# Performance work log

Hardware: AMD Instinct MI355X
Metric: run time of the kernel (lower is better)

Reference implementation:

```python
import jax, jax.numpy as jnp
import numpy as np

B, T, D, H = 4, 4096, 2048, 128

def setup_inputs() -> dict:
    key = jax.random.key(0)
    k1, k2, k3, k4 = jax.random.split(key, 4)
    scale = 0.02
    return {
        "x": jax.random.normal(k1, (B, T, D), dtype=jnp.float32),
        "Wq": jax.random.normal(k2, (D, H), dtype=jnp.float32) * scale,
        "Wk": jax.random.normal(k3, (D, H), dtype=jnp.float32) * scale,
        "Wv": jax.random.normal(k4, (D, H), dtype=jnp.float32) * scale,
    }

def reference(x, Wq, Wk, Wv):
    # x: [B,T,D]; projections to [B,T,H]
    q = jnp.einsum('btd,dh->bth', x, Wq)
    k = jnp.einsum('btd,dh->bth', x, Wk)
    v = jnp.einsum('btd,dh->bth', x, Wv)
    scale = 1.0 / jnp.sqrt(jnp.asarray(q.shape[-1], q.dtype))
    scores = jnp.einsum('bth,bsh->bts', q, k) * scale  # [B,T,T]
    t = x.shape[1]
    causal = jnp.tril(jnp.ones((t, t), dtype=bool))
    scores = jnp.where(causal, scores, -jnp.inf)
    weights = jax.nn.softmax(scores, axis=-1)
    # dropout p=0.0 (eval) -> identity
    out = jnp.einsum('bts,bsh->bth', weights, v)
    return out
```

## Files before the change

kernel.cpp:

```cpp
#include <hip/hip_runtime.h>
#include <hip/hip_bf16.h>

#define Bq 4
#define Tq 4096
#define Dq 2048
#define Hq 128
#define Mq (Bq*Tq)
#define CHUNK 16

typedef __attribute__((ext_vector_type(8))) short bf16x8;
typedef __attribute__((ext_vector_type(4))) float f32x4;

static __device__ __forceinline__ short bfbits(float f) {
    union { __hip_bfloat16 h; short s; } u;
    u.h = __float2bfloat16(f);
    return u.s;
}
static __device__ __forceinline__ float bf2f(short s) {
    union { unsigned u; float f; } v;
    v.u = ((unsigned)(unsigned short)s) << 16;
    return v.f;
}
#define WAIT_LDS() __builtin_amdgcn_s_waitcnt(0xC07F)

static __device__ __forceinline__ void gload16(const void* g, void* l) {
    __builtin_amdgcn_global_load_lds(
        (const __attribute__((address_space(1))) unsigned int*)g,
        (__attribute__((address_space(3))) unsigned int*)l, 16, 0, 0);
}

__global__ __launch_bounds__(256, 1) void wt_kernel(
    const float* __restrict__ Wqp,
    const float* __restrict__ Wkp,
    const float* __restrict__ Wvp,
    short* __restrict__ wTg)
{
    __shared__ short trsp[128][136];
    const int kc = blockIdx.x;
    const int w  = blockIdx.y;
    const float* __restrict__ W = (w == 0) ? Wqp : (w == 1) ? Wkp : Wvp;
    const float scale = (w == 0) ? 0.08838834764831843f : 1.0f;
    const int t = threadIdx.x;

    #pragma unroll
    for (int i = 0; i < 16; i++) {
        int idx = t + i * 256;
        int r = idx >> 5, c4 = idx & 31;
        float4 f = *(const float4*)&W[(size_t)(kc * 128 + r) * Hq + c4 * 4];
        trsp[c4 * 4 + 0][r] = bfbits(f.x * scale);
        trsp[c4 * 4 + 1][r] = bfbits(f.y * scale);
        trsp[c4 * 4 + 2][r] = bfbits(f.z * scale);
        trsp[c4 * 4 + 3][r] = bfbits(f.w * scale);
    }
    __syncthreads();
    #pragma unroll
    for (int i = 0; i < 8; i++) {
        int idx = t + i * 256;
        int h = idx >> 4, c8 = idx & 15;
        *(bf16x8*)&wTg[((size_t)w * 128 + h) * Dq + kc * 128 + c8 * 8] =
            *(bf16x8*)&trsp[h][c8 * 8];
    }
}

__global__ __launch_bounds__(512, 2) void qkv_fused_kernel(
    const float* __restrict__ x,
    const short* __restrict__ wTg,
    short* __restrict__ qg,
    short* __restrict__ kg,
    short* __restrict__ vTt)
{
    __shared__ __attribute__((aligned(128))) char smem[114688];

    const int bid  = blockIdx.x;
    const int mi   = bid & 127;
    const int ni   = bid >> 7;
    const int m0   = mi * 128;
    const int n0   = ni * 192;

    const int t    = threadIdx.x;
    const int l    = t & 63;
    const int w    = t >> 6;
    const int l15  = l & 15;
    const int quad = l >> 4;
    const int wmi  = w & 3;
    const int wni  = w >> 2;
    const int swzA = l15 << 4;
    const int swzB = (l15 & 7) << 4;

    f32x4 o[2][6];
    #pragma unroll
    for (int mf = 0; mf < 2; mf++)
        #pragma unroll
        for (int j = 0; j < 6; j++) o[mf][j] = (f32x4){0.f, 0.f, 0.f, 0.f};

    const short* wsrc0 = wTg + (size_t)(n0 + 24 * w + (l >> 3)) * Dq
                             + (((l & 7) ^ (l >> 3)) << 3);

    #define ISSUE(it2, par)                                                      \
        do {                                                                     \
            char* wb_ = smem + (par) * 24576;                                    \
            _Pragma("unroll")                                                    \
            for (int j = 0; j < 3; j++)                                          \
                gload16(wsrc0 + (size_t)j * 8 * Dq + (it2) * 64,                 \
                        wb_ + (w * 3 + j) * 1024);                               \
            char* xb_ = smem + 49152 + (par) * 32768;                            \
            _Pragma("unroll")                                                    \
            for (int j = 0; j < 4; j++) {                                        \
                int row_ = 16 * w + 4 * j + (l >> 4);                            \
                int col_ = ((l & 15) ^ (4 * j + (l >> 4))) << 2;                 \
                gload16(x + (size_t)(m0 + row_) * Dq + (it2) * 64 + col_,        \
                        xb_ + (w * 4 + j) * 1024);                               \
            }                                                                    \
        } while (0)

    #define COMPUTE(par)                                                         \
        do {                                                                     \
            const char* wb_ = smem + (par) * 24576;                              \
            const char* xb_ = smem + 49152 + (par) * 32768;                      \
            _Pragma("unroll")                                                    \
            for (int kk = 0; kk < 2; kk++) {                                     \
                bf16x8 a[2], b[6];                                               \
                _Pragma("unroll")                                                \
                for (int mf = 0; mf < 2; mf++) {                                 \
                    const char* rp = xb_ + (wmi * 32 + mf * 16 + l15) * 256;     \
                    const int kb = kk * 128 + quad * 32;                         \
                    f32x4 f0 = *(const f32x4*)(rp + ((kb     ) ^ swzA));         \
                    f32x4 f1 = *(const f32x4*)(rp + ((kb + 16) ^ swzA));         \
                    bf16x8 af;                                                   \
                    af[0] = bfbits(f0[0]); af[1] = bfbits(f0[1]);                \
                    af[2] = bfbits(f0[2]); af[3] = bfbits(f0[3]);                \
                    af[4] = bfbits(f1[0]); af[5] = bfbits(f1[1]);                \
                    af[6] = bfbits(f1[2]); af[7] = bfbits(f1[3]);                \
                    a[mf] = af;                                                  \
                }                                                                \
                _Pragma("unroll")                                                \
                for (int j = 0; j < 6; j++)                                      \
                    b[j] = *(const bf16x8*)(wb_ + (wni * 96 + j * 16 + l15) * 128\
                                                + ((kk * 64 + quad * 16) ^ swzB));\
                _Pragma("unroll")                                                \
                for (int mf = 0; mf < 2; mf++)                                   \
                    _Pragma("unroll")                                            \
                    for (int j = 0; j < 6; j++)                                  \
                        o[mf][j] = __builtin_amdgcn_mfma_f32_16x16x32_bf16(      \
                            a[mf], b[j], o[mf][j], 0, 0, 0);                     \
            }                                                                    \
        } while (0)

    ISSUE(0, 0);
    ISSUE(1, 1);

    #pragma unroll 1
    for (int it = 0; it < 32; ++it) {
        if (it < 31) asm volatile("s_waitcnt vmcnt(7)" ::: "memory");
        else         asm volatile("s_waitcnt vmcnt(0)" ::: "memory");
        __builtin_amdgcn_s_barrier();
        __builtin_amdgcn_sched_barrier(0);
        COMPUTE(it & 1);
        __builtin_amdgcn_s_barrier();
        __builtin_amdgcn_sched_barrier(0);
        if (it < 30) ISSUE(it + 2, it & 1);
    }

    #undef COMPUTE
    #undef ISSUE

    {
        short (*e)[200] = (short(*)[200])smem;
        #pragma unroll
        for (int mf = 0; mf < 2; mf++)
            #pragma unroll
            for (int j = 0; j < 6; j++) {
                int nloc = wni * 96 + j * 16;
                if (n0 + nloc < 256) {
                    #pragma unroll
                    for (int reg = 0; reg < 4; reg++)
                        e[wmi * 32 + mf * 16 + quad * 4 + reg][nloc + l15] =
                            bfbits(o[mf][j][reg]);
                }
            }
        __syncthreads();
        const int r  = t >> 2;
        const int u0 = (t & 3) * 6;
        #pragma unroll
        for (int i = 0; i < 6; i++) {
            int u  = u0 + i;
            int ng = n0 + u * 8;
            if (ng < 256) {
                bf16x8 val = *(bf16x8*)&e[r][u * 8];
                short* dst = (ng < 128) ? &qg[(size_t)(m0 + r) * Hq + ng]
                                        : &kg[(size_t)(m0 + r) * Hq + (ng - 128)];
                *(bf16x8*)dst = val;
            }
        }
    }
    if (ni == 1) {
        __syncthreads();
        short (*ev)[136] = (short(*)[136])(smem + 53248);
        #pragma unroll
        for (int mf = 0; mf < 2; mf++)
            #pragma unroll
            for (int j = 0; j < 6; j++) {
                int nloc = wni * 96 + j * 16;
                if (nloc >= 64) {
                    short4 pk;
                    pk.x = bfbits(o[mf][j][0]); pk.y = bfbits(o[mf][j][1]);
                    pk.z = bfbits(o[mf][j][2]); pk.w = bfbits(o[mf][j][3]);
                    *(short4*)&ev[(nloc - 64) + l15][wmi * 32 + mf * 16 + quad * 4] = pk;
                }
            }
        __syncthreads();
        const int bb  = m0 / Tq;
        const int jt0 = (m0 % Tq) >> 6;
        #pragma unroll
        for (int i = 0; i < 4; i++) {
            int idx = t + i * 512;
            int h = idx >> 4, u = idx & 15;
            int m = u * 8;
            int jt = jt0 + (m >> 6);
            *(bf16x8*)&vTt[(((size_t)bb * (Tq / 64) + jt) * 128 + h) * 64 + (m & 63)] =
                *(bf16x8*)&ev[h][m];
        }
    }
}

__global__ __launch_bounds__(256, 3) void attn_part_kernel(
    const short* __restrict__ qg, const short* __restrict__ kg,
    const short* __restrict__ vTt,
    short* __restrict__ Opart,
    float* __restrict__ lv)
{
    __shared__ short ks_s[64][136];
    __shared__ short vt_s[128][72];
    __shared__ short ps_s[64][72];

    const int qt = blockIdx.x;
    const int b  = blockIdx.y;
    const int c  = blockIdx.z;
    const int q0 = qt * 64;

    const int lo = c * CHUNK;
    const int hi = min(qt + 1, lo + CHUNK);
    if (lo >= hi) return;

    const int t    = threadIdx.x;
    const int lane = t & 63;
    const int qw   = t >> 6;
    const int l15  = lane & 15;
    const int quad = lane >> 4;

    bf16x8 qf[4];
    {
        const short* qsrc = qg + (size_t)(b * Tq + q0 + qw * 16 + l15) * Hq + quad * 8;
        #pragma unroll
        for (int kk = 0; kk < 4; kk++)
            qf[kk] = *(const bf16x8*)(qsrc + kk * 32);
    }

    float lsum[4] = {0.f, 0.f, 0.f, 0.f};
    f32x4 o[8];
    #pragma unroll
    for (int nf = 0; nf < 8; nf++) o[nf] = (f32x4){0.f, 0.f, 0.f, 0.f};

    bf16x8 kreg[4], vreg[4];
    {
        const size_t kbase = (size_t)(b * Tq + lo * 64) * Hq;
        const short* vsrc = vTt + (((size_t)b * (Tq / 64) + lo) * 128) * 64;
        #pragma unroll
        for (int i = 0; i < 4; i++) {
            int idx = t + i * 256;
            kreg[i] = *(const bf16x8*)&kg[kbase + (size_t)(idx >> 4) * Hq + (idx & 15) * 8];
            vreg[i] = *(const bf16x8*)&vsrc[idx * 8];
        }
        #pragma unroll
        for (int i = 0; i < 4; i++) {
            int idx = t + i * 256;
            *(bf16x8*)&ks_s[idx >> 4][(idx & 15) * 8] = kreg[i];
            *(bf16x8*)&vt_s[idx >> 3][(idx & 7) * 8]  = vreg[i];
        }
    }
    __syncthreads();

    for (int jt = lo; jt < hi; jt++) {
        if (jt + 1 < hi) {
            const size_t kbase = (size_t)(b * Tq + (jt + 1) * 64) * Hq;
            const short* vsrc = vTt + (((size_t)b * (Tq / 64) + jt + 1) * 128) * 64;
            #pragma unroll
            for (int i = 0; i < 4; i++) {
                int idx = t + i * 256;
                kreg[i] = *(const bf16x8*)&kg[kbase + (size_t)(idx >> 4) * Hq + (idx & 15) * 8];
                vreg[i] = *(const bf16x8*)&vsrc[idx * 8];
            }
        }

        f32x4 sacc[4];
        #pragma unroll
        for (int nf = 0; nf < 4; nf++) sacc[nf] = (f32x4){0.f, 0.f, 0.f, 0.f};
        #pragma unroll
        for (int kk = 0; kk < 4; kk++) {
            bf16x8 bk[4];
            #pragma unroll
            for (int nf = 0; nf < 4; nf++)
                bk[nf] = *(bf16x8*)&ks_s[nf * 16 + l15][kk * 32 + quad * 8];
            #pragma unroll
            for (int nf = 0; nf < 4; nf++)
                sacc[nf] = __builtin_amdgcn_mfma_f32_16x16x32_bf16(qf[kk], bk[nf], sacc[nf], 0, 0, 0);
        }

        const bool diag = (jt == qt);
        #pragma unroll
        for (int reg = 0; reg < 4; reg++) {
            const int rloc = qw * 16 + quad * 4 + reg;
            #pragma unroll
            for (int nf = 0; nf < 4; nf++) {
                float s = sacc[nf][reg];
                if (diag && (nf * 16 + l15 > rloc)) s = -1e30f;
                float p = __expf(s);
                lsum[reg] += p;
                ps_s[rloc][nf * 16 + l15] = bfbits(p);
            }
        }
        WAIT_LDS();

        #pragma unroll
        for (int ks2 = 0; ks2 < 2; ks2++) {
            bf16x8 ap = *(bf16x8*)&ps_s[qw * 16 + l15][ks2 * 32 + quad * 8];
            bf16x8 bv[8];
            #pragma unroll
            for (int nf = 0; nf < 8; nf++)
                bv[nf] = *(bf16x8*)&vt_s[nf * 16 + l15][ks2 * 32 + quad * 8];
            #pragma unroll
            for (int nf = 0; nf < 8; nf++)
                o[nf] = __builtin_amdgcn_mfma_f32_16x16x32_bf16(ap, bv[nf], o[nf], 0, 0, 0);
        }

        __syncthreads();
        if (jt + 1 < hi) {
            #pragma unroll
            for (int i = 0; i < 4; i++) {
                int idx = t + i * 256;
                *(bf16x8*)&ks_s[idx >> 4][(idx & 15) * 8] = kreg[i];
                *(bf16x8*)&vt_s[idx >> 3][(idx & 7) * 8]  = vreg[i];
            }
            __syncthreads();
        }
    }

    #pragma unroll
    for (int reg = 0; reg < 4; reg++) {
        #pragma unroll
        for (int mm = 8; mm >= 1; mm >>= 1)
            lsum[reg] += __shfl_xor(lsum[reg], mm, 16);
    }
    const size_t zoff = (size_t)c * Mq;
    if (l15 == 0) {
        #pragma unroll
        for (int reg = 0; reg < 4; reg++)
            lv[zoff + (size_t)b * Tq + q0 + qw * 16 + quad * 4 + reg] = lsum[reg];
    }

    __syncthreads();
    short (*epi)[136] = (short(*)[136])&ks_s[0][0];
    #pragma unroll
    for (int nf = 0; nf < 8; nf++)
        #pragma unroll
        for (int reg = 0; reg < 4; reg++)
            epi[qw * 16 + quad * 4 + reg][nf * 16 + l15] = bfbits(o[nf][reg]);
    __syncthreads();
    #pragma unroll
    for (int i = 0; i < 4; i++) {
        int idx = t + i * 256;
        int r = idx >> 4, cc = idx & 15;
        *(bf16x8*)&Opart[(zoff + (size_t)b * Tq + q0 + r) * Hq + cc * 8] =
            *(bf16x8*)&epi[r][cc * 8];
    }
}

__global__ __launch_bounds__(256, 4) void merge_kernel(
    const short* __restrict__ Opart, const float* __restrict__ lv,
    float* __restrict__ outg)
{
    const int t   = threadIdx.x;
    const int row = blockIdx.x * 16 + (t >> 4);
    const int cu  = t & 15;

    const int rl  = row & (Tq - 1);
    const int nch = (rl >> 10) + 1;

    float lsum = 0.f;
    float acc[8] = {};
    for (int cc = 0; cc < nch; cc++) {
        lsum += lv[(size_t)cc * Mq + row];
        bf16x8 oc = *(const bf16x8*)&Opart[((size_t)cc * Mq + row) * Hq + cu * 8];
        #pragma unroll
        for (int j = 0; j < 8; j++) acc[j] += bf2f(oc[j]);
    }
    float inv = 1.0f / lsum;

    float4 r0, r1;
    r0.x = acc[0] * inv; r0.y = acc[1] * inv; r0.z = acc[2] * inv; r0.w = acc[3] * inv;
    r1.x = acc[4] * inv; r1.y = acc[5] * inv; r1.z = acc[6] * inv; r1.w = acc[7] * inv;
    float* dst = &outg[(size_t)row * Hq + cu * 8];
    *(float4*)dst       = r0;
    *(float4*)(dst + 4) = r1;
}

extern "C" void kernel_launch(void* const* d_in, const int* in_sizes, int n_in,
                              void* d_out, int out_size, void* d_ws, size_t ws_size,
                              hipStream_t stream) {
    const float* x   = (const float*)d_in[0];
    const float* Wqp = (const float*)d_in[1];
    const float* Wkp = (const float*)d_in[2];
    const float* Wvp = (const float*)d_in[3];
    float* out = (float*)d_out;

    short* qg    = (short*)d_ws;
    short* kg    = qg  + (size_t)Mq * Hq;
    short* vTt   = kg  + (size_t)Mq * Hq;
    short* Opart = vTt + (size_t)Mq * Hq;
    short* wTg   = Opart;
    float* lv    = (float*)(Opart + (size_t)4 * Mq * Hq);

    wt_kernel<<<dim3(16, 3), dim3(256), 0, stream>>>(Wqp, Wkp, Wvp, wTg);
    qkv_fused_kernel<<<dim3(256), dim3(512), 0, stream>>>(x, wTg, qg, kg, vTt);
    attn_part_kernel<<<dim3(Tq / 64, Bq, 4), dim3(256), 0, stream>>>(qg, kg, vTt, Opart, lv);
    merge_kernel<<<dim3(Mq / 16), dim3(256), 0, stream>>>(Opart, lv, out);
}
```

Measured before the change: 265.2 us.

## Stage QKV projection loads through registers and convert x to bf16 before LDS

The QKV projection GEMM no longer uses direct global-to-LDS loads. x and W tiles are now loaded into registers two iterations ahead, x is converted to bf16 once per element, and the packed bf16 data is written to swizzled LDS. This halves the LDS footprint for x (114688 to 81920 bytes) and removes the repeated fp32-to-bf16 conversion the consumer waves did in the MFMA loop. In exchange it adds register pressure, costs VGPR-to-LDS write instructions, and changes the barrier and waitcnt schedule, with an unrolled two-stage loop and epilogue.

```diff
diff --git a/kernel.cpp b/kernel.cpp
--- a/kernel.cpp
+++ b/kernel.cpp
@@ -21,13 +21,11 @@
     v.u = ((unsigned)(unsigned short)s) << 16;
     return v.f;
 }
+static __device__ __forceinline__ unsigned pk2(float a, float b) {
+    return ((unsigned)(unsigned short)bfbits(a)) |
+           (((unsigned)(unsigned short)bfbits(b)) << 16);
+}
 #define WAIT_LDS() __builtin_amdgcn_s_waitcnt(0xC07F)
-
-static __device__ __forceinline__ void gload16(const void* g, void* l) {
-    __builtin_amdgcn_global_load_lds(
-        (const __attribute__((address_space(1))) unsigned int*)g,
-        (__attribute__((address_space(3))) unsigned int*)l, 16, 0, 0);
-}
 
 __global__ __launch_bounds__(256, 1) void wt_kernel(
     const float* __restrict__ Wqp,
@@ -69,7 +67,7 @@
     short* __restrict__ kg,
     short* __restrict__ vTt)
 {
-    __shared__ __attribute__((aligned(128))) char smem[114688];
+    __shared__ __attribute__((aligned(128))) char smem[81920];
 
     const int bid  = blockIdx.x;
     const int mi   = bid & 127;
@@ -84,8 +82,7 @@
     const int quad = l >> 4;
     const int wmi  = w & 3;
     const int wni  = w >> 2;
-    const int swzA = l15 << 4;
-    const int swzB = (l15 & 7) << 4;
+    const int swz  = (l15 & 7) << 4;
 
     f32x4 o[2][6];
     #pragma unroll
@@ -93,50 +90,56 @@
         #pragma unroll
         for (int j = 0; j < 6; j++) o[mf][j] = (f32x4){0.f, 0.f, 0.f, 0.f};
 
-    const short* wsrc0 = wTg + (size_t)(n0 + 24 * w + (l >> 3)) * Dq
-                             + (((l & 7) ^ (l >> 3)) << 3);
-
-    #define ISSUE(it2, par)                                                      \
+    const float* xsrc = x + (size_t)(m0 + (t >> 4)) * Dq + (t & 15) * 4;
+    const short* wsrc = wTg + (size_t)(n0 + (t >> 3)) * Dq + (t & 7) * 8;
+    const int xwb0 = (t >> 4) * 128 + (((t & 15) << 3) ^ (((t >> 4) & 7) << 4));
+    const int wwb0 = (t >> 3) * 128 + (((t & 7) << 4) ^ (((t >> 3) & 7) << 4));
+
+    float4  xg[2][4];
+    bf16x8  wg[2][3];
+
+    #define LOAD(it2, s)                                                         \
+        do {                                                                     \
+            _Pragma("unroll")                                                    \
+            for (int j = 0; j < 4; j++)                                          \
+                xg[s][j] = *(const float4*)(xsrc + (size_t)j * 32 * Dq + (it2) * 64); \
+            _Pragma("unroll")                                                    \
+            for (int j = 0; j < 3; j++)                                          \
+                wg[s][j] = *(const bf16x8*)(wsrc + (size_t)j * 64 * Dq + (it2) * 64); \
+        } while (0)
+
+    #define WRITE(par, s)                                                        \
         do {                                                                     \
             char* wb_ = smem + (par) * 24576;                                    \
+            char* xb_ = smem + 49152 + (par) * 16384;                            \
+            _Pragma("unroll")                                                    \
+            for (int j = 0; j < 4; j++) {                                        \
+                uint2 u;                                                         \
+                u.x = pk2(xg[s][j].x, xg[s][j].y);                               \
+                u.y = pk2(xg[s][j].z, xg[s][j].w);                               \
+                *(uint2*)(xb_ + xwb0 + j * 4096) = u;                            \
+            }                                                                    \
             _Pragma("unroll")                                                    \
             for (int j = 0; j < 3; j++)                                          \
-                gload16(wsrc0 + (size_t)j * 8 * Dq + (it2) * 64,                 \
-                        wb_ + (w * 3 + j) * 1024);                               \
-            char* xb_ = smem + 49152 + (par) * 32768;                            \
-            _Pragma("unroll")                                                    \
-            for (int j = 0; j < 4; j++) {                                        \
-                int row_ = 16 * w + 4 * j + (l >> 4);                            \
-                int col_ = ((l & 15) ^ (4 * j + (l >> 4))) << 2;                 \
-                gload16(x + (size_t)(m0 + row_) * Dq + (it2) * 64 + col_,        \
-                        xb_ + (w * 4 + j) * 1024);                               \
-            }                                                                    \
+                *(bf16x8*)(wb_ + wwb0 + j * 8192) = wg[s][j];                    \
         } while (0)
 
     #define COMPUTE(par)                                                         \
         do {                                                                     \
             const char* wb_ = smem + (par) * 24576;                              \
-            const char* xb_ = smem + 49152 + (par) * 32768;                      \
+            const char* xb_ = smem + 49152 + (par) * 16384;                      \
             _Pragma("unroll")                                                    \
             for (int kk = 0; kk < 2; kk++) {                                     \
+                const int kb = kk * 64 + quad * 16;                              \
                 bf16x8 a[2], b[6];                                               \
                 _Pragma("unroll")                                                \
-                for (int mf = 0; mf < 2; mf++) {                                 \
-                    const char* rp = xb_ + (wmi * 32 + mf * 16 + l15) * 256;     \
-                    const int kb = kk * 128 + quad * 32;                         \
-                    f32x4 f0 = *(const f32x4*)(rp + ((kb     ) ^ swzA));         \
-                    f32x4 f1 = *(const f32x4*)(rp + ((kb + 16) ^ swzA));         \
-                    bf16x8 af;                                                   \
-                    af[0] = bfbits(f0[0]); af[1] = bfbits(f0[1]);                \
-                    af[2] = bfbits(f0[2]); af[3] = bfbits(f0[3]);                \
-                    af[4] = bfbits(f1[0]); af[5] = bfbits(f1[1]);                \
-                    af[6] = bfbits(f1[2]); af[7] = bfbits(f1[3]);                \
-                    a[mf] = af;                                                  \
-                }                                                                \
+                for (int mf = 0; mf < 2; mf++)                                   \
+                    a[mf] = *(const bf16x8*)(xb_ + (wmi * 32 + mf * 16 + l15) * 128 \
+                                                 + (kb ^ swz));                  \
                 _Pragma("unroll")                                                \
                 for (int j = 0; j < 6; j++)                                      \
                     b[j] = *(const bf16x8*)(wb_ + (wni * 96 + j * 16 + l15) * 128\
-                                                + ((kk * 64 + quad * 16) ^ swzB));\
+                                                + (kb ^ swz));                   \
                 _Pragma("unroll")                                                \
                 for (int mf = 0; mf < 2; mf++)                                   \
                     _Pragma("unroll")                                            \
@@ -146,23 +149,46 @@
             }                                                                    \
         } while (0)
 
-    ISSUE(0, 0);
-    ISSUE(1, 1);
+    #define BODY(it, p)                                                          \
+        do {                                                                     \
+            asm volatile("s_waitcnt lgkmcnt(0)" ::: "memory");                   \
+            __builtin_amdgcn_s_barrier();                                        \
+            __builtin_amdgcn_sched_barrier(0);                                   \
+            LOAD((it) + 2, p);                                                   \
+            COMPUTE(p);                                                          \
+            asm volatile("s_waitcnt vmcnt(7)" ::: "memory");                     \
+            __builtin_amdgcn_sched_barrier(0);                                   \
+            WRITE(1 - (p), 1 - (p));                                             \
+        } while (0)
+
+    LOAD(0, 0);
+    LOAD(1, 1);
+    asm volatile("s_waitcnt vmcnt(7)" ::: "memory");
+    __builtin_amdgcn_sched_barrier(0);
+    WRITE(0, 0);
 
     #pragma unroll 1
-    for (int it = 0; it < 32; ++it) {
-        if (it < 31) asm volatile("s_waitcnt vmcnt(7)" ::: "memory");
-        else         asm volatile("s_waitcnt vmcnt(0)" ::: "memory");
-        __builtin_amdgcn_s_barrier();
-        __builtin_amdgcn_sched_barrier(0);
-        COMPUTE(it & 1);
-        __builtin_amdgcn_s_barrier();
-        __builtin_amdgcn_sched_barrier(0);
-        if (it < 30) ISSUE(it + 2, it & 1);
-    }
-
+    for (int itp = 0; itp < 15; itp++) {
+        BODY(itp * 2,     0);
+        BODY(itp * 2 + 1, 1);
+    }
+    asm volatile("s_waitcnt lgkmcnt(0)" ::: "memory");
+    __builtin_amdgcn_s_barrier();
+    __builtin_amdgcn_sched_barrier(0);
+    COMPUTE(0);
+    asm volatile("s_waitcnt vmcnt(0)" ::: "memory");
+    __builtin_amdgcn_sched_barrier(0);
+    WRITE(1, 1);
+    asm volatile("s_waitcnt lgkmcnt(0)" ::: "memory");
+    __builtin_amdgcn_s_barrier();
+    __builtin_amdgcn_sched_barrier(0);
+    COMPUTE(1);
+    __builtin_amdgcn_s_barrier();
+
+    #undef BODY
     #undef COMPUTE
-    #undef ISSUE
+    #undef WRITE
+    #undef LOAD
 
     {
         short (*e)[200] = (short(*)[200])smem;
@@ -195,7 +221,7 @@
     }
     if (ni == 1) {
         __syncthreads();
-        short (*ev)[136] = (short(*)[136])(smem + 53248);
+        short (*ev)[136] = (short(*)[136])smem;
         #pragma unroll
         for (int mf = 0; mf < 2; mf++)
             #pragma unroll
```

Result: slower. 285.9 us (+7.8%).

## Replace LDS-staged QKV GEMM with direct global loads and split-K across waves

Applied to the files above, without the earlier changes.

The QKV projection kernel no longer stages x and W tiles through LDS with async global_load_lds and double buffering. Each wave now loads its MFMA operands straight from global memory into registers. The K dimension is split across wave pairs, and the two partial results are combined through a small LDS reduction before the epilogue. This removes LDS traffic, the per-iteration barriers and a large LDS footprint, at the cost of uncoalesced, latency-exposed global loads, no explicit prefetch, and a doubled per-wave accumulator register set.

```diff
diff --git a/kernel.cpp b/kernel.cpp
--- a/kernel.cpp
+++ b/kernel.cpp
@@ -22,12 +22,6 @@
     return v.f;
 }
 #define WAIT_LDS() __builtin_amdgcn_s_waitcnt(0xC07F)
-
-static __device__ __forceinline__ void gload16(const void* g, void* l) {
-    __builtin_amdgcn_global_load_lds(
-        (const __attribute__((address_space(1))) unsigned int*)g,
-        (__attribute__((address_space(3))) unsigned int*)l, 16, 0, 0);
-}
 
 __global__ __launch_bounds__(256, 1) void wt_kernel(
     const float* __restrict__ Wqp,
@@ -69,7 +63,7 @@
     short* __restrict__ kg,
     short* __restrict__ vTt)
 {
-    __shared__ __attribute__((aligned(128))) char smem[114688];
+    __shared__ __attribute__((aligned(128))) char smem[51200];
 
     const int bid  = blockIdx.x;
     const int mi   = bid & 127;
@@ -82,102 +76,88 @@
     const int w    = t >> 6;
     const int l15  = l & 15;
     const int quad = l >> 4;
-    const int wmi  = w & 3;
-    const int wni  = w >> 2;
-    const int swzA = l15 << 4;
-    const int swzB = (l15 & 7) << 4;
-
-    f32x4 o[2][6];
-    #pragma unroll
-    for (int mf = 0; mf < 2; mf++)
+    const int wm   = (w >> 2) & 1;
+    const int wk   = (w >> 1) & 1;
+    const int wn   = w & 1;
+
+    const float* xp = x + (size_t)(m0 + wm * 64 + l15) * Dq + wk * 1024 + quad * 8;
+    const short* wp = wTg + (size_t)(n0 + wn * 96 + l15) * Dq + wk * 1024 + quad * 8;
+
+    f32x4 o[4][6];
+    #pragma unroll
+    for (int mf = 0; mf < 4; mf++)
         #pragma unroll
         for (int j = 0; j < 6; j++) o[mf][j] = (f32x4){0.f, 0.f, 0.f, 0.f};
 
-    const short* wsrc0 = wTg + (size_t)(n0 + 24 * w + (l >> 3)) * Dq
-                             + (((l & 7) ^ (l >> 3)) << 3);
-
-    #define ISSUE(it2, par)                                                      \
-        do {                                                                     \
-            char* wb_ = smem + (par) * 24576;                                    \
-            _Pragma("unroll")                                                    \
-            for (int j = 0; j < 3; j++)                                          \
-                gload16(wsrc0 + (size_t)j * 8 * Dq + (it2) * 64,                 \
-                        wb_ + (w * 3 + j) * 1024);                               \
-            char* xb_ = smem + 49152 + (par) * 32768;                            \
-            _Pragma("unroll")                                                    \
-            for (int j = 0; j < 4; j++) {                                        \
-                int row_ = 16 * w + 4 * j + (l >> 4);                            \
-                int col_ = ((l & 15) ^ (4 * j + (l >> 4))) << 2;                 \
-                gload16(x + (size_t)(m0 + row_) * Dq + (it2) * 64 + col_,        \
-                        xb_ + (w * 4 + j) * 1024);                               \
-            }                                                                    \
-        } while (0)
-
-    #define COMPUTE(par)                                                         \
-        do {                                                                     \
-            const char* wb_ = smem + (par) * 24576;                              \
-            const char* xb_ = smem + 49152 + (par) * 32768;                      \
-            _Pragma("unroll")                                                    \
-            for (int kk = 0; kk < 2; kk++) {                                     \
-                bf16x8 a[2], b[6];                                               \
-                _Pragma("unroll")                                                \
-                for (int mf = 0; mf < 2; mf++) {                                 \
-                    const char* rp = xb_ + (wmi * 32 + mf * 16 + l15) * 256;     \
-                    const int kb = kk * 128 + quad * 32;                         \
-                    f32x4 f0 = *(const f32x4*)(rp + ((kb     ) ^ swzA));         \
-                    f32x4 f1 = *(const f32x4*)(rp + ((kb + 16) ^ swzA));         \
-                    bf16x8 af;                                                   \
-                    af[0] = bfbits(f0[0]); af[1] = bfbits(f0[1]);                \
-                    af[2] = bfbits(f0[2]); af[3] = bfbits(f0[3]);                \
-                    af[4] = bfbits(f1[0]); af[5] = bfbits(f1[1]);                \
-                    af[6] = bfbits(f1[2]); af[7] = bfbits(f1[3]);                \
-                    a[mf] = af;                                                  \
-                }                                                                \
-                _Pragma("unroll")                                                \
-                for (int j = 0; j < 6; j++)                                      \
-                    b[j] = *(const bf16x8*)(wb_ + (wni * 96 + j * 16 + l15) * 128\
-                                                + ((kk * 64 + quad * 16) ^ swzB));\
-                _Pragma("unroll")                                                \
-                for (int mf = 0; mf < 2; mf++)                                   \
-                    _Pragma("unroll")                                            \
-                    for (int j = 0; j < 6; j++)                                  \
-                        o[mf][j] = __builtin_amdgcn_mfma_f32_16x16x32_bf16(      \
-                            a[mf], b[j], o[mf][j], 0, 0, 0);                     \
-            }                                                                    \
-        } while (0)
-
-    ISSUE(0, 0);
-    ISSUE(1, 1);
-
-    #pragma unroll 1
+    #pragma unroll 2
     for (int it = 0; it < 32; ++it) {
-        if (it < 31) asm volatile("s_waitcnt vmcnt(7)" ::: "memory");
-        else         asm volatile("s_waitcnt vmcnt(0)" ::: "memory");
-        __builtin_amdgcn_s_barrier();
-        __builtin_amdgcn_sched_barrier(0);
-        COMPUTE(it & 1);
-        __builtin_amdgcn_s_barrier();
-        __builtin_amdgcn_sched_barrier(0);
-        if (it < 30) ISSUE(it + 2, it & 1);
-    }
-
-    #undef COMPUTE
-    #undef ISSUE
+        const int k0 = it * 32;
+        bf16x8 a[4];
+        #pragma unroll
+        for (int mf = 0; mf < 4; mf++) {
+            float4 f0 = *(const float4*)(xp + (size_t)mf * 16 * Dq + k0);
+            float4 f1 = *(const float4*)(xp + (size_t)mf * 16 * Dq + k0 + 4);
+            bf16x8 af;
+            af[0] = bfbits(f0.x); af[1] = bfbits(f0.y);
+            af[2] = bfbits(f0.z); af[3] = bfbits(f0.w);
+            af[4] = bfbits(f1.x); af[5] = bfbits(f1.y);
+            af[6] = bfbits(f1.z); af[7] = bfbits(f1.w);
+            a[mf] = af;
+        }
+        bf16x8 b[6];
+        #pragma unroll
+        for (int j = 0; j < 6; j++)
+            b[j] = *(const bf16x8*)(wp + (size_t)j * 16 * Dq + k0);
+        #pragma unroll
+        for (int mf = 0; mf < 4; mf++)
+            #pragma unroll
+            for (int j = 0; j < 6; j++)
+                o[mf][j] = __builtin_amdgcn_mfma_f32_16x16x32_bf16(
+                    a[mf], b[j], o[mf][j], 0, 0, 0);
+    }
+
+    {
+        float* cmb = (float*)smem;
+        const int widx = wm * 2 + wn;
+        #pragma unroll
+        for (int p = 0; p < 2; p++) {
+            if (wk == 1) {
+                #pragma unroll
+                for (int mf = 0; mf < 4; mf++)
+                    #pragma unroll
+                    for (int jj = 0; jj < 3; jj++)
+                        *(f32x4*)&cmb[(((widx * 64 + l) * 12) + mf * 3 + jj) * 4] =
+                            o[mf][p * 3 + jj];
+            }
+            __syncthreads();
+            if (wk == 0) {
+                #pragma unroll
+                for (int mf = 0; mf < 4; mf++)
+                    #pragma unroll
+                    for (int jj = 0; jj < 3; jj++)
+                        o[mf][p * 3 + jj] +=
+                            *(const f32x4*)&cmb[(((widx * 64 + l) * 12) + mf * 3 + jj) * 4];
+            }
+            __syncthreads();
+        }
+    }
 
     {
         short (*e)[200] = (short(*)[200])smem;
-        #pragma unroll
-        for (int mf = 0; mf < 2; mf++)
-            #pragma unroll
-            for (int j = 0; j < 6; j++) {
-                int nloc = wni * 96 + j * 16;
-                if (n0 + nloc < 256) {
-                    #pragma unroll
-                    for (int reg = 0; reg < 4; reg++)
-                        e[wmi * 32 + mf * 16 + quad * 4 + reg][nloc + l15] =
-                            bfbits(o[mf][j][reg]);
+        if (wk == 0) {
+            #pragma unroll
+            for (int mf = 0; mf < 4; mf++)
+                #pragma unroll
+                for (int j = 0; j < 6; j++) {
+                    int nloc = wn * 96 + j * 16;
+                    if (n0 + nloc < 256) {
+                        #pragma unroll
+                        for (int reg = 0; reg < 4; reg++)
+                            e[wm * 64 + mf * 16 + quad * 4 + reg][nloc + l15] =
+                                bfbits(o[mf][j][reg]);
+                    }
                 }
-            }
+        }
         __syncthreads();
         const int r  = t >> 2;
         const int u0 = (t & 3) * 6;
@@ -195,19 +175,21 @@
     }
     if (ni == 1) {
         __syncthreads();
-        short (*ev)[136] = (short(*)[136])(smem + 53248);
-        #pragma unroll
-        for (int mf = 0; mf < 2; mf++)
-            #pragma unroll
-            for (int j = 0; j < 6; j++) {
-                int nloc = wni * 96 + j * 16;
-                if (nloc >= 64) {
-                    short4 pk;
-                    pk.x = bfbits(o[mf][j][0]); pk.y = bfbits(o[mf][j][1]);
-                    pk.z = bfbits(o[mf][j][2]); pk.w = bfbits(o[mf][j][3]);
-                    *(short4*)&ev[(nloc - 64) + l15][wmi * 32 + mf * 16 + quad * 4] = pk;
+        short (*ev)[136] = (short(*)[136])smem;
+        if (wk == 0) {
+            #pragma unroll
+            for (int mf = 0; mf < 4; mf++)
+                #pragma unroll
+                for (int j = 0; j < 6; j++) {
+                    int nloc = wn * 96 + j * 16;
+                    if (nloc >= 64) {
+                        short4 pk;
+                        pk.x = bfbits(o[mf][j][0]); pk.y = bfbits(o[mf][j][1]);
+                        pk.z = bfbits(o[mf][j][2]); pk.w = bfbits(o[mf][j][3]);
+                        *(short4*)&ev[(nloc - 64) + l15][wm * 64 + mf * 16 + quad * 4] = pk;
+                    }
                 }
-            }
+        }
         __syncthreads();
         const int bb  = m0 / Tq;
         const int jt0 = (m0 % Tq) >> 6;
```

Measured after the change: 343.3 us. +29.4%, slower.
